# Kernel tuning notes

Measured on AMD Instinct MI355X. Metric: run time of the kernel, lower is better.

## Reference

```python
import jax, jax.numpy as jnp
import numpy as np

B, T, C = 2, 2048, 1024
N_HEAD = 16
HEAD_DIM = C // N_HEAD


def setup_inputs() -> dict:
    key = jax.random.key(0)
    ks = jax.random.split(key, 5)
    s = 0.02
    return {
        "x": jax.random.normal(ks[0], (B, T, C), dtype=jnp.float32),
        "W_kqv": jax.random.normal(ks[1], (C, 3 * C), dtype=jnp.float32) * s,
        "b_kqv": jax.random.normal(ks[2], (3 * C,), dtype=jnp.float32) * s,
        "W_proj": jax.random.normal(ks[3], (C, C), dtype=jnp.float32) * s,
        "b_proj": jax.random.normal(ks[4], (C,), dtype=jnp.float32) * s,
    }


def reference(x, W_kqv, b_kqv, W_proj, b_proj):
    Bx, Tx, Cx = x.shape
    qkv = x @ W_kqv + b_kqv                      # [B, T, 3C]
    q, k, v = jnp.split(qkv, 3, axis=-1)
    # [B, H, T, D]
    q = q.reshape(Bx, Tx, N_HEAD, HEAD_DIM).transpose(0, 2, 1, 3)
    k = k.reshape(Bx, Tx, N_HEAD, HEAD_DIM).transpose(0, 2, 1, 3)
    v = v.reshape(Bx, Tx, N_HEAD, HEAD_DIM).transpose(0, 2, 1, 3)
    scale = 1.0 / jnp.sqrt(jnp.asarray(HEAD_DIM, dtype=x.dtype))
    att = jnp.einsum("bhqd,bhkd->bhqk", q, k) * scale  # [B, H, T, T]
    causal = jnp.tril(jnp.ones((Tx, Tx), dtype=bool))   # [T, T]
    att = jnp.where(causal[None, None], att, jnp.float32(-jnp.inf))
    att = jax.nn.softmax(att, axis=-1)
    y = jnp.einsum("bhqk,bhkd->bhqd", att, v)            # [B, H, T, D]
    y = y.transpose(0, 2, 1, 3).reshape(Bx, Tx, Cx)
    out = y @ W_proj + b_proj
    return out, k, v
```

## Files before the change

kernel.cpp:

```cpp
#include <hip/hip_runtime.h>


#define DEVI __device__ __forceinline__

typedef unsigned short ushort_t;
typedef unsigned long long u64_t;
typedef __attribute__((ext_vector_type(4))) unsigned short us4;
typedef __attribute__((ext_vector_type(8))) unsigned short ushort8;
typedef __attribute__((ext_vector_type(4))) float f32x4;
typedef __attribute__((ext_vector_type(8))) __bf16 bf16x8;

DEVI unsigned short f2bf(float f) {
  union { float f; unsigned int u; } c; c.f = f;
  unsigned int u = c.u;
  unsigned int r = (u + 0x7FFFu + ((u >> 16) & 1u)) >> 16;
  return (unsigned short)r;
}

DEVI float exp2v(float x) {
  float r;
  asm("v_exp_f32 %0, %1\n\ts_nop 0" : "=v"(r) : "v"(x));
  return r;
}

DEVI unsigned int cvtpk(float lo, float hi) {
  unsigned int r;
  asm("v_cvt_pk_bf16_f32 %0, %1, %2" : "=v"(r) : "v"(lo), "v"(hi));
  return r;
}

DEVI f32x4 mfma16(ushort8 a, ushort8 b, f32x4 c) {
  return __builtin_amdgcn_mfma_f32_16x16x32_bf16(
      __builtin_bit_cast(bf16x8, a), __builtin_bit_cast(bf16x8, b), c, 0, 0, 0);
}

typedef const __attribute__((address_space(1))) void* gptr_t;
typedef __attribute__((address_space(3))) void* lptr_t;
#define GLOAD_LDS16(g, l) \
  __builtin_amdgcn_global_load_lds((gptr_t)(g), (lptr_t)(l), 16, 0, 0)

DEVI void bar() {
  asm volatile("" ::: "memory");
  __builtin_amdgcn_s_barrier();
  asm volatile("" ::: "memory");
}
#define VMCNT(n) asm volatile("s_waitcnt vmcnt(" #n ")" ::: "memory")


__global__ void prep_kernel(const float* __restrict__ x,
                            const float* __restrict__ Wk,
                            const float* __restrict__ Wp,
                            ushort_t* __restrict__ Xb,
                            ushort_t* __restrict__ Wkt,
                            ushort_t* __restrict__ Wpt) {
  __shared__ float tile[32][33];
  const int id = blockIdx.x, tid = threadIdx.x;
  if (id < 2048) {
    const int i = id * 256 + tid;
    const f32x4* p = (const f32x4*)x;
    f32x4 a = p[2 * i], b = p[2 * i + 1];
    ushort8 o;
    o[0] = f2bf(a[0]); o[1] = f2bf(a[1]); o[2] = f2bf(a[2]); o[3] = f2bf(a[3]);
    o[4] = f2bf(b[0]); o[5] = f2bf(b[1]); o[6] = f2bf(b[2]); o[7] = f2bf(b[3]);
    ((ushort8*)Xb)[i] = o;
    return;
  }
  const float* in;
  ushort_t* outp;
  int R = 1024, Cin, bx, by;
  if (id < 5120) {
    const int jid = id - 2048;
    bx = jid % 96; by = jid / 96; in = Wk; outp = Wkt; Cin = 3072;
  } else {
    const int jid = id - 5120;
    bx = jid % 32; by = jid / 32; in = Wp; outp = Wpt; Cin = 1024;
  }
  const int c0 = bx * 32, r0 = by * 32;
  const int tx = tid & 31, ty = tid >> 5;
#pragma unroll
  for (int it = 0; it < 4; ++it)
    tile[ty + it * 8][tx] = in[(size_t)(r0 + ty + it * 8) * Cin + c0 + tx];
  __syncthreads();
#pragma unroll
  for (int it = 0; it < 4; ++it)
    outp[(size_t)(c0 + ty + it * 8) * R + r0 + tx] = f2bf(tile[tx][ty + it * 8]);
}


__global__ __launch_bounds__(256) void gemm_bt_kernel(
    const ushort_t* __restrict__ A, const ushort_t* __restrict__ Bt,
    const float* __restrict__ bias, float* __restrict__ outF,
    float* __restrict__ outK, float* __restrict__ outV,
    ushort_t* __restrict__ Qb, ushort_t* __restrict__ Kb, ushort_t* __restrict__ Vb,
    int M, int N, int K, int mode) {
  __shared__ __align__(16) ushort_t As[128 * 64];
  __shared__ __align__(16) ushort_t Bs[128 * 64];
  const int tid = threadIdx.x;
  const int w = tid >> 6, lane = tid & 63;
  const int wr = w >> 1, wc = w & 1;
  const int nby = gridDim.y;
  const int chy = nby >> 3;
  const int orig = blockIdx.x + gridDim.x * blockIdx.y;
  const int xcd = orig & 7, idx = orig >> 3;
  const int by = xcd * chy + (idx % chy);
  const int bx = idx / chy;
  const int m0 = by * 128, n0 = bx * 128;
  const int l15 = lane & 15, lhi = lane >> 4;
  const int rowA = lane >> 3;
  const int sgc = (((lane & 7) ^ ((lane >> 3) & 7)) << 3);

  f32x4 acc[4][4] = {};

  const int nk = K >> 6;
  for (int kt = 0; kt < nk; ++kt) {
    const size_t k0 = (size_t)kt << 6;
    if (kt) bar();
#pragma unroll
    for (int it = 0; it < 4; ++it) {
      const int rbase = (w * 4 + it) * 8;
      GLOAD_LDS16(A + (size_t)(m0 + rbase + rowA) * K + k0 + sgc, &As[rbase * 64]);
      GLOAD_LDS16(Bt + (size_t)(n0 + rbase + rowA) * K + k0 + sgc, &Bs[rbase * 64]);
    }
    VMCNT(0);
    bar();
#pragma unroll
    for (int kk = 0; kk < 2; ++kk) {
      const int gof = (((kk * 4 + lhi) ^ (l15 & 7)) << 3);
      ushort8 a[4], b[4];
#pragma unroll
      for (int i = 0; i < 4; ++i)
        a[i] = *(const ushort8*)&As[(wr * 64 + i * 16 + l15) * 64 + gof];
#pragma unroll
      for (int j = 0; j < 4; ++j)
        b[j] = *(const ushort8*)&Bs[(wc * 64 + j * 16 + l15) * 64 + gof];
#pragma unroll
      for (int i = 0; i < 4; ++i)
#pragma unroll
        for (int j = 0; j < 4; ++j) acc[i][j] = mfma16(a[i], b[j], acc[i][j]);
    }
  }

  const float QSCALE = 0.18033688011112042f;
#pragma unroll
  for (int i = 0; i < 4; ++i) {
#pragma unroll
    for (int j = 0; j < 4; ++j) {
      const int nn = n0 + wc * 64 + j * 16 + l15;
      const float bv = bias[nn];
#pragma unroll
      for (int r = 0; r < 4; ++r) {
        const int mm = m0 + wr * 64 + i * 16 + lhi * 4 + r;
        const float v = acc[i][j][r] + bv;
        if (mode == 0) {
          outF[(size_t)mm * N + nn] = v;
        } else {
          const int bb = mm >> 11, t = mm & 2047;
          const int c = nn & 1023, h = c >> 6, d = c & 63;
          const size_t idx2 = ((size_t)(bb * 16 + h) * 2048 + t) * 64 + d;
          const int sec = nn >> 10;
          if (sec == 0) {
            Qb[idx2] = f2bf(v * QSCALE);
          } else if (sec == 1) {
            outK[idx2] = v; Kb[idx2] = f2bf(v);
          } else {
            outV[idx2] = v; Vb[idx2] = f2bf(v);
          }
        }
      }
    }
  }
}


__global__ __launch_bounds__(256) void gemm_bt64_kernel(
    const ushort_t* __restrict__ A, const ushort_t* __restrict__ Bt,
    const float* __restrict__ bias, float* __restrict__ outF,
    int M, int N, int K) {
  __shared__ __align__(16) ushort_t As[64 * 64];
  __shared__ __align__(16) ushort_t Bs[128 * 64];
  const int tid = threadIdx.x;
  const int w = tid >> 6, lane = tid & 63;
  const int wr = w >> 1, wc = w & 1;
  const int nby = gridDim.y;
  const int chy = nby >> 3;
  const int orig = blockIdx.x + gridDim.x * blockIdx.y;
  const int xcd = orig & 7, idx = orig >> 3;
  const int by = xcd * chy + (idx % chy);
  const int bx = idx / chy;
  const int m0 = by * 64, n0 = bx * 128;
  const int l15 = lane & 15, lhi = lane >> 4;
  const int rowA = lane >> 3;
  const int sgc = (((lane & 7) ^ ((lane >> 3) & 7)) << 3);

  f32x4 acc[2][4] = {};

  const int nk = K >> 6;
  for (int kt = 0; kt < nk; ++kt) {
    const size_t k0 = (size_t)kt << 6;
    if (kt) bar();
#pragma unroll
    for (int it = 0; it < 2; ++it) {
      const int rbase = (w * 2 + it) * 8;
      GLOAD_LDS16(A + (size_t)(m0 + rbase + rowA) * K + k0 + sgc, &As[rbase * 64]);
    }
#pragma unroll
    for (int it = 0; it < 4; ++it) {
      const int rbase = (w * 4 + it) * 8;
      GLOAD_LDS16(Bt + (size_t)(n0 + rbase + rowA) * K + k0 + sgc, &Bs[rbase * 64]);
    }
    VMCNT(0);
    bar();
#pragma unroll
    for (int kk = 0; kk < 2; ++kk) {
      const int gof = (((kk * 4 + lhi) ^ (l15 & 7)) << 3);
      ushort8 a[2], b[4];
#pragma unroll
      for (int i = 0; i < 2; ++i)
        a[i] = *(const ushort8*)&As[(wr * 32 + i * 16 + l15) * 64 + gof];
#pragma unroll
      for (int j = 0; j < 4; ++j)
        b[j] = *(const ushort8*)&Bs[(wc * 64 + j * 16 + l15) * 64 + gof];
#pragma unroll
      for (int i = 0; i < 2; ++i)
#pragma unroll
        for (int j = 0; j < 4; ++j) acc[i][j] = mfma16(a[i], b[j], acc[i][j]);
    }
  }

#pragma unroll
  for (int i = 0; i < 2; ++i) {
#pragma unroll
    for (int j = 0; j < 4; ++j) {
      const int nn = n0 + wc * 64 + j * 16 + l15;
      const float bv = bias[nn];
#pragma unroll
      for (int r = 0; r < 4; ++r) {
        const int mm = m0 + wr * 32 + i * 16 + lhi * 4 + r;
        outF[(size_t)mm * N + nn] = acc[i][j][r] + bv;
      }
    }
  }
}


__global__ __launch_bounds__(512) void attn_kernel(
    const ushort_t* __restrict__ Qb, const ushort_t* __restrict__ Kb,
    const ushort_t* __restrict__ Vb, ushort_t* __restrict__ Yb) {
  __shared__ __align__(16) ushort_t Ks[2][64 * 64];
  __shared__ __align__(16) ushort_t Vt[2][64 * 72];
  __shared__ __align__(16) ushort_t Pl[8 * 16 * 72];
  const int id = blockIdx.x;
  const int xcd = id & 7;
  int qt, bh;
  if (id < 256) {
    const int j = id >> 3;
    bh = xcd + 8 * (j & 3);
    qt = 8 + (j >> 2);
  } else {
    const int j = (id - 256) >> 3;
    bh = xcd + 8 * (j & 3);
    qt = 7 - (j >> 2);
  }
  const int b = bh >> 4, h = bh & 15;
  const int tid = threadIdx.x, w = tid >> 6, lane = tid & 63;
  const int l15 = lane & 15, lhi = lane >> 4;
  const int swzP = 2 * (l15 & 3);
  const size_t base = (size_t)bh * 2048 * 64;
  const float NEG_INF = -__builtin_inff();
  ushort_t* myP = &Pl[w * 16 * 72];

  const int krow = tid >> 3, kg = tid & 7;
  const int ksg = kg ^ (krow & 7);
  const int vd0 = (tid & 15) * 4;
  const int vt0 = (tid >> 4) * 2;

  const int nkt = 2 * qt + 2;
  const int qrow = w * 16 + l15;

  ushort8 qf[2];
  {
    const size_t qrg = base + (size_t)(qt * 128 + qrow) * 64;
    qf[0] = *(const ushort8*)&Qb[qrg + lhi * 8];
    qf[1] = *(const ushort8*)&Qb[qrg + 32 + lhi * 8];
  }
  float m_s = NEG_INF, l_s = 0.f;
  f32x4 o[4] = {};

  {
    GLOAD_LDS16(Kb + base + (size_t)krow * 64 + ksg * 8, &Ks[0][tid * 8]);
    const ushort_t* vp = Vb + base + (size_t)vt0 * 64 + vd0;
    u64_t a = *(const u64_t*)vp;
    u64_t c = *(const u64_t*)(vp + 64);
    us4 av = __builtin_bit_cast(us4, a);
    us4 cv = __builtin_bit_cast(us4, c);
#pragma unroll
    for (int i = 0; i < 4; ++i) {
      const int d = vd0 + i;
      const int scg = (vt0 >> 3) ^ ((d >> 3) & 7);
      unsigned int wv = (unsigned int)av[i] | ((unsigned int)cv[i] << 16);
      *(unsigned int*)&Vt[0][d * 72 + scg * 8 + (vt0 & 7)] = wv;
    }
  }
  __syncthreads();

  for (int kt = 0; kt < nkt; ++kt) {
    const int cur = kt & 1, nxt = cur ^ 1;
    const bool pf = (kt + 1 < nkt);
    u64_t va = 0, vc = 0;
    if (pf) {
      const size_t tb = base + (size_t)(kt + 1) * 64 * 64;
      GLOAD_LDS16(Kb + tb + (size_t)krow * 64 + ksg * 8, &Ks[nxt][tid * 8]);
      const ushort_t* vp = Vb + tb + (size_t)vt0 * 64 + vd0;
      va = *(const u64_t*)vp;
      vc = *(const u64_t*)(vp + 64);
    }

    f32x4 s[4] = {};
#pragma unroll
    for (int kk = 0; kk < 2; ++kk) {
#pragma unroll
      for (int j = 0; j < 4; ++j) {
        const int g = (kk * 4 + lhi) ^ (l15 & 7);
        ushort8 kb = *(const ushort8*)&Ks[cur][(j * 16 + l15) * 64 + g * 8];
        s[j] = mfma16(kb, qf[kk], s[j]);
      }
    }
    if (64 * kt + 63 > 128 * qt + w * 16) {
      const int delta = 128 * qt + qrow - 64 * kt;
#pragma unroll
      for (int j = 0; j < 4; ++j)
#pragma unroll
        for (int r = 0; r < 4; ++r)
          if ((j * 16 + lhi * 4 + r) > delta) s[j][r] = NEG_INF;
    }

    float pmax = s[0][0];
#pragma unroll
    for (int j = 0; j < 4; ++j)
#pragma unroll
      for (int r = 0; r < 4; ++r) pmax = fmaxf(pmax, s[j][r]);
    pmax = fmaxf(pmax, __shfl_xor(pmax, 16));
    pmax = fmaxf(pmax, __shfl_xor(pmax, 32));
    if (__any(pmax - m_s > 8.0f)) {
      const float mnew = fmaxf(m_s, pmax);
      const float al = exp2v(m_s - mnew);
      m_s = mnew;
      l_s *= al;
#pragma unroll
      for (int df = 0; df < 4; ++df)
#pragma unroll
        for (int r = 0; r < 4; ++r) o[df][r] *= al;
    }
    float rsum = 0.f;
#pragma unroll
    for (int j = 0; j < 4; ++j)
#pragma unroll
      for (int r = 0; r < 4; ++r) {
        const float pe = exp2v(s[j][r] - m_s);
        s[j][r] = pe;
        rsum += pe;
      }
    rsum += __shfl_xor(rsum, 16);
    rsum += __shfl_xor(rsum, 32);
    l_s += rsum;

#pragma unroll
    for (int j = 0; j < 4; ++j) {
      const unsigned int w0 = cvtpk(s[j][0], s[j][1]);
      const unsigned int w1 = cvtpk(s[j][2], s[j][3]);
      const u64_t dw = (u64_t)w0 | ((u64_t)w1 << 32);
      const int cg = j * 2 + (lhi >> 1);
      *(u64_t*)&myP[l15 * 72 + ((cg ^ swzP) << 3) + ((lhi & 1) << 2)] = dw;
    }

#pragma unroll
    for (int kk = 0; kk < 2; ++kk) {
      ushort8 pa = *(const ushort8*)&myP[l15 * 72 + (((kk * 4 + lhi) ^ swzP) << 3)];
#pragma unroll
      for (int df = 0; df < 4; ++df) {
        const int r = df * 16 + l15;
        const int g = (kk * 4 + lhi) ^ ((r >> 3) & 7);
        ushort8 vb = *(const ushort8*)&Vt[cur][r * 72 + g * 8];
        o[df] = mfma16(vb, pa, o[df]);
      }
    }

    if (pf) {
      us4 av = __builtin_bit_cast(us4, va);
      us4 cv = __builtin_bit_cast(us4, vc);
#pragma unroll
      for (int i = 0; i < 4; ++i) {
        const int d = vd0 + i;
        const int scg = (vt0 >> 3) ^ ((d >> 3) & 7);
        unsigned int wv = (unsigned int)av[i] | ((unsigned int)cv[i] << 16);
        *(unsigned int*)&Vt[nxt][d * 72 + scg * 8 + (vt0 & 7)] = wv;
      }
    }
    __syncthreads();
  }

  const float inv = 1.0f / l_s;
  const size_t yrow = (size_t)(b * 2048 + qt * 128 + qrow) * 1024 + h * 64;
#pragma unroll
  for (int df = 0; df < 4; ++df) {
    us4 ov;
#pragma unroll
    for (int r = 0; r < 4; ++r) ov[r] = f2bf(o[df][r] * inv);
    *(us4*)&Yb[yrow + df * 16 + lhi * 4] = ov;
  }
}


extern "C" void kernel_launch(void* const* d_in, const int* in_sizes, int n_in,
                              void* d_out, int out_size, void* d_ws, size_t ws_size,
                              hipStream_t stream) {
  const float* x      = (const float*)d_in[0];
  const float* W_kqv  = (const float*)d_in[1];
  const float* b_kqv  = (const float*)d_in[2];
  const float* W_proj = (const float*)d_in[3];
  const float* b_proj = (const float*)d_in[4];
  float* out  = (float*)d_out;
  float* outK = out + 4194304;
  float* outV = out + 8388608;

  char* ws = (char*)d_ws;
  ushort_t* Xb  = (ushort_t*)(ws);
  ushort_t* Wkt = (ushort_t*)(ws + ((size_t)8 << 20));
  ushort_t* Wpt = (ushort_t*)(ws + ((size_t)14 << 20));
  ushort_t* Qb  = (ushort_t*)(ws + ((size_t)16 << 20));
  ushort_t* Kb  = (ushort_t*)(ws + ((size_t)24 << 20));
  ushort_t* Vb  = (ushort_t*)(ws + ((size_t)32 << 20));
  ushort_t* Yb  = Xb;

  prep_kernel<<<6144, 256, 0, stream>>>(x, W_kqv, W_proj, Xb, Wkt, Wpt);
  gemm_bt_kernel<<<dim3(24, 32), 256, 0, stream>>>(
      Xb, Wkt, b_kqv, nullptr, outK, outV, Qb, Kb, Vb, 4096, 3072, 1024, 1);
  attn_kernel<<<512, 512, 0, stream>>>(Qb, Kb, Vb, Yb);
  gemm_bt64_kernel<<<dim3(8, 64), 256, 0, stream>>>(
      Yb, Wpt, b_proj, out, 4096, 1024, 1024);
}
```

Before: 106.7 us.

## Halve attention block to 4 waves, each handling two 16-row query groups

The attention kernel now runs 256 threads per block instead of 512. Each wave owns 32 query rows as two 16-row groups, so every K and V fragment read from LDS feeds two MFMAs, and the wave keeps two sets of softmax state. The K/V tile loads are split across two iterations per thread, and the V transpose swizzle changes from (d>>3) to (d>>2). The aim is to cut LDS read traffic per MFMA, at the cost of more registers per wave and fewer waves per block to hide latency.

```diff
diff --git a/kernel.cpp b/kernel.cpp
--- a/kernel.cpp
+++ b/kernel.cpp
@@ -243,7 +243,7 @@
 }
 
 
-__global__ __launch_bounds__(512) void attn_kernel(
+__global__ __launch_bounds__(256) void attn_kernel(
     const ushort_t* __restrict__ Qb, const ushort_t* __restrict__ Kb,
     const ushort_t* __restrict__ Vb, ushort_t* __restrict__ Yb) {
   __shared__ __align__(16) ushort_t Ks[2][64 * 64];
@@ -267,38 +267,46 @@
   const int swzP = 2 * (l15 & 3);
   const size_t base = (size_t)bh * 2048 * 64;
   const float NEG_INF = -__builtin_inff();
-  ushort_t* myP = &Pl[w * 16 * 72];
-
-  const int krow = tid >> 3, kg = tid & 7;
-  const int ksg = kg ^ (krow & 7);
+  ushort_t* myP = &Pl[w * 2 * 16 * 72];
+
   const int vd0 = (tid & 15) * 4;
-  const int vt0 = (tid >> 4) * 2;
+  const int vt0b = (tid >> 4) * 2;
 
   const int nkt = 2 * qt + 2;
-  const int qrow = w * 16 + l15;
-
-  ushort8 qf[2];
+
+  ushort8 qf[2][2];
+#pragma unroll
+  for (int qg = 0; qg < 2; ++qg) {
+    const size_t qrg = base + (size_t)(qt * 128 + w * 32 + qg * 16 + l15) * 64;
+    qf[qg][0] = *(const ushort8*)&Qb[qrg + lhi * 8];
+    qf[qg][1] = *(const ushort8*)&Qb[qrg + 32 + lhi * 8];
+  }
+  float m_s[2] = {NEG_INF, NEG_INF}, l_s[2] = {0.f, 0.f};
+  f32x4 o[2][4] = {};
+
   {
-    const size_t qrg = base + (size_t)(qt * 128 + qrow) * 64;
-    qf[0] = *(const ushort8*)&Qb[qrg + lhi * 8];
-    qf[1] = *(const ushort8*)&Qb[qrg + 32 + lhi * 8];
-  }
-  float m_s = NEG_INF, l_s = 0.f;
-  f32x4 o[4] = {};
-
-  {
-    GLOAD_LDS16(Kb + base + (size_t)krow * 64 + ksg * 8, &Ks[0][tid * 8]);
-    const ushort_t* vp = Vb + base + (size_t)vt0 * 64 + vd0;
-    u64_t a = *(const u64_t*)vp;
-    u64_t c = *(const u64_t*)(vp + 64);
-    us4 av = __builtin_bit_cast(us4, a);
-    us4 cv = __builtin_bit_cast(us4, c);
-#pragma unroll
-    for (int i = 0; i < 4; ++i) {
-      const int d = vd0 + i;
-      const int scg = (vt0 >> 3) ^ ((d >> 3) & 7);
-      unsigned int wv = (unsigned int)av[i] | ((unsigned int)cv[i] << 16);
-      *(unsigned int*)&Vt[0][d * 72 + scg * 8 + (vt0 & 7)] = wv;
+#pragma unroll
+    for (int it = 0; it < 2; ++it) {
+      const int chunk = tid + it * 256;
+      const int row = chunk >> 3, g = chunk & 7;
+      const int sg = g ^ (row & 7);
+      GLOAD_LDS16(Kb + base + (size_t)row * 64 + sg * 8, &Ks[0][chunk * 8]);
+    }
+#pragma unroll
+    for (int it = 0; it < 2; ++it) {
+      const int t0 = vt0b + it * 32;
+      const ushort_t* vp = Vb + base + (size_t)t0 * 64 + vd0;
+      u64_t a = *(const u64_t*)vp;
+      u64_t c = *(const u64_t*)(vp + 64);
+      us4 av = __builtin_bit_cast(us4, a);
+      us4 cv = __builtin_bit_cast(us4, c);
+#pragma unroll
+      for (int i = 0; i < 4; ++i) {
+        const int d = vd0 + i;
+        const int scg = (t0 >> 3) ^ ((d >> 2) & 7);
+        unsigned int wv = (unsigned int)av[i] | ((unsigned int)cv[i] << 16);
+        *(unsigned int*)&Vt[0][d * 72 + scg * 8 + (t0 & 7)] = wv;
+      }
     }
   }
   __syncthreads();
@@ -306,107 +314,133 @@
   for (int kt = 0; kt < nkt; ++kt) {
     const int cur = kt & 1, nxt = cur ^ 1;
     const bool pf = (kt + 1 < nkt);
-    u64_t va = 0, vc = 0;
+    u64_t va[2], vc[2];
     if (pf) {
       const size_t tb = base + (size_t)(kt + 1) * 64 * 64;
-      GLOAD_LDS16(Kb + tb + (size_t)krow * 64 + ksg * 8, &Ks[nxt][tid * 8]);
-      const ushort_t* vp = Vb + tb + (size_t)vt0 * 64 + vd0;
-      va = *(const u64_t*)vp;
-      vc = *(const u64_t*)(vp + 64);
-    }
-
-    f32x4 s[4] = {};
+#pragma unroll
+      for (int it = 0; it < 2; ++it) {
+        const int chunk = tid + it * 256;
+        const int row = chunk >> 3, g = chunk & 7;
+        const int sg = g ^ (row & 7);
+        GLOAD_LDS16(Kb + tb + (size_t)row * 64 + sg * 8, &Ks[nxt][chunk * 8]);
+      }
+#pragma unroll
+      for (int it = 0; it < 2; ++it) {
+        const int t0 = vt0b + it * 32;
+        const ushort_t* vp = Vb + tb + (size_t)t0 * 64 + vd0;
+        va[it] = *(const u64_t*)vp;
+        vc[it] = *(const u64_t*)(vp + 64);
+      }
+    }
+
+    f32x4 s[2][4] = {};
 #pragma unroll
     for (int kk = 0; kk < 2; ++kk) {
 #pragma unroll
       for (int j = 0; j < 4; ++j) {
         const int g = (kk * 4 + lhi) ^ (l15 & 7);
         ushort8 kb = *(const ushort8*)&Ks[cur][(j * 16 + l15) * 64 + g * 8];
-        s[j] = mfma16(kb, qf[kk], s[j]);
-      }
-    }
-    if (64 * kt + 63 > 128 * qt + w * 16) {
-      const int delta = 128 * qt + qrow - 64 * kt;
+        s[0][j] = mfma16(kb, qf[0][kk], s[0][j]);
+        s[1][j] = mfma16(kb, qf[1][kk], s[1][j]);
+      }
+    }
+
+#pragma unroll
+    for (int qg = 0; qg < 2; ++qg) {
+      const int qrow = w * 32 + qg * 16 + l15;
+      if (64 * kt + 63 > 128 * qt + w * 32 + qg * 16) {
+        const int delta = 128 * qt + qrow - 64 * kt;
+#pragma unroll
+        for (int j = 0; j < 4; ++j)
+#pragma unroll
+          for (int r = 0; r < 4; ++r)
+            if ((j * 16 + lhi * 4 + r) > delta) s[qg][j][r] = NEG_INF;
+      }
+      float pmax = s[qg][0][0];
 #pragma unroll
       for (int j = 0; j < 4; ++j)
 #pragma unroll
-        for (int r = 0; r < 4; ++r)
-          if ((j * 16 + lhi * 4 + r) > delta) s[j][r] = NEG_INF;
-    }
-
-    float pmax = s[0][0];
-#pragma unroll
-    for (int j = 0; j < 4; ++j)
-#pragma unroll
-      for (int r = 0; r < 4; ++r) pmax = fmaxf(pmax, s[j][r]);
-    pmax = fmaxf(pmax, __shfl_xor(pmax, 16));
-    pmax = fmaxf(pmax, __shfl_xor(pmax, 32));
-    if (__any(pmax - m_s > 8.0f)) {
-      const float mnew = fmaxf(m_s, pmax);
-      const float al = exp2v(m_s - mnew);
-      m_s = mnew;
-      l_s *= al;
-#pragma unroll
-      for (int df = 0; df < 4; ++df)
-#pragma unroll
-        for (int r = 0; r < 4; ++r) o[df][r] *= al;
-    }
-    float rsum = 0.f;
-#pragma unroll
-    for (int j = 0; j < 4; ++j)
-#pragma unroll
-      for (int r = 0; r < 4; ++r) {
-        const float pe = exp2v(s[j][r] - m_s);
-        s[j][r] = pe;
-        rsum += pe;
-      }
-    rsum += __shfl_xor(rsum, 16);
-    rsum += __shfl_xor(rsum, 32);
-    l_s += rsum;
-
-#pragma unroll
-    for (int j = 0; j < 4; ++j) {
-      const unsigned int w0 = cvtpk(s[j][0], s[j][1]);
-      const unsigned int w1 = cvtpk(s[j][2], s[j][3]);
-      const u64_t dw = (u64_t)w0 | ((u64_t)w1 << 32);
-      const int cg = j * 2 + (lhi >> 1);
-      *(u64_t*)&myP[l15 * 72 + ((cg ^ swzP) << 3) + ((lhi & 1) << 2)] = dw;
+        for (int r = 0; r < 4; ++r) pmax = fmaxf(pmax, s[qg][j][r]);
+      pmax = fmaxf(pmax, __shfl_xor(pmax, 16));
+      pmax = fmaxf(pmax, __shfl_xor(pmax, 32));
+      if (__any(pmax - m_s[qg] > 8.0f)) {
+        const float mnew = fmaxf(m_s[qg], pmax);
+        const float al = exp2v(m_s[qg] - mnew);
+        m_s[qg] = mnew;
+        l_s[qg] *= al;
+#pragma unroll
+        for (int df = 0; df < 4; ++df)
+#pragma unroll
+          for (int r = 0; r < 4; ++r) o[qg][df][r] *= al;
+      }
+      float rsum = 0.f;
+#pragma unroll
+      for (int j = 0; j < 4; ++j)
+#pragma unroll
+        for (int r = 0; r < 4; ++r) {
+          const float pe = exp2v(s[qg][j][r] - m_s[qg]);
+          s[qg][j][r] = pe;
+          rsum += pe;
+        }
+      rsum += __shfl_xor(rsum, 16);
+      rsum += __shfl_xor(rsum, 32);
+      l_s[qg] += rsum;
+
+      ushort_t* pq = myP + qg * 16 * 72;
+#pragma unroll
+      for (int j = 0; j < 4; ++j) {
+        const unsigned int w0 = cvtpk(s[qg][j][0], s[qg][j][1]);
+        const unsigned int w1 = cvtpk(s[qg][j][2], s[qg][j][3]);
+        const u64_t dw = (u64_t)w0 | ((u64_t)w1 << 32);
+        const int cg = j * 2 + (lhi >> 1);
+        *(u64_t*)&pq[l15 * 72 + ((cg ^ swzP) << 3) + ((lhi & 1) << 2)] = dw;
+      }
     }
 
 #pragma unroll
     for (int kk = 0; kk < 2; ++kk) {
-      ushort8 pa = *(const ushort8*)&myP[l15 * 72 + (((kk * 4 + lhi) ^ swzP) << 3)];
+      ushort8 pa0 = *(const ushort8*)&myP[l15 * 72 + (((kk * 4 + lhi) ^ swzP) << 3)];
+      ushort8 pa1 = *(const ushort8*)&myP[16 * 72 + l15 * 72 + (((kk * 4 + lhi) ^ swzP) << 3)];
 #pragma unroll
       for (int df = 0; df < 4; ++df) {
         const int r = df * 16 + l15;
-        const int g = (kk * 4 + lhi) ^ ((r >> 3) & 7);
+        const int g = (kk * 4 + lhi) ^ ((r >> 2) & 7);
         ushort8 vb = *(const ushort8*)&Vt[cur][r * 72 + g * 8];
-        o[df] = mfma16(vb, pa, o[df]);
+        o[0][df] = mfma16(vb, pa0, o[0][df]);
+        o[1][df] = mfma16(vb, pa1, o[1][df]);
       }
     }
 
     if (pf) {
-      us4 av = __builtin_bit_cast(us4, va);
-      us4 cv = __builtin_bit_cast(us4, vc);
-#pragma unroll
-      for (int i = 0; i < 4; ++i) {
-        const int d = vd0 + i;
-        const int scg = (vt0 >> 3) ^ ((d >> 3) & 7);
-        unsigned int wv = (unsigned int)av[i] | ((unsigned int)cv[i] << 16);
-        *(unsigned int*)&Vt[nxt][d * 72 + scg * 8 + (vt0 & 7)] = wv;
+#pragma unroll
+      for (int it = 0; it < 2; ++it) {
+        const int t0 = vt0b + it * 32;
+        us4 av = __builtin_bit_cast(us4, va[it]);
+        us4 cv = __builtin_bit_cast(us4, vc[it]);
+#pragma unroll
+        for (int i = 0; i < 4; ++i) {
+          const int d = vd0 + i;
+          const int scg = (t0 >> 3) ^ ((d >> 2) & 7);
+          unsigned int wv = (unsigned int)av[i] | ((unsigned int)cv[i] << 16);
+          *(unsigned int*)&Vt[nxt][d * 72 + scg * 8 + (t0 & 7)] = wv;
+        }
       }
     }
     __syncthreads();
   }
 
-  const float inv = 1.0f / l_s;
-  const size_t yrow = (size_t)(b * 2048 + qt * 128 + qrow) * 1024 + h * 64;
-#pragma unroll
-  for (int df = 0; df < 4; ++df) {
-    us4 ov;
-#pragma unroll
-    for (int r = 0; r < 4; ++r) ov[r] = f2bf(o[df][r] * inv);
-    *(us4*)&Yb[yrow + df * 16 + lhi * 4] = ov;
+#pragma unroll
+  for (int qg = 0; qg < 2; ++qg) {
+    const float inv = 1.0f / l_s[qg];
+    const size_t yrow =
+        (size_t)(b * 2048 + qt * 128 + w * 32 + qg * 16 + l15) * 1024 + h * 64;
+#pragma unroll
+    for (int df = 0; df < 4; ++df) {
+      us4 ov;
+#pragma unroll
+      for (int r = 0; r < 4; ++r) ov[r] = f2bf(o[qg][df][r] * inv);
+      *(us4*)&Yb[yrow + df * 16 + lhi * 4] = ov;
+    }
   }
 }
 
@@ -435,7 +469,7 @@
   prep_kernel<<<6144, 256, 0, stream>>>(x, W_kqv, W_proj, Xb, Wkt, Wpt);
   gemm_bt_kernel<<<dim3(24, 32), 256, 0, stream>>>(
       Xb, Wkt, b_kqv, nullptr, outK, outV, Qb, Kb, Vb, 4096, 3072, 1024, 1);
-  attn_kernel<<<512, 512, 0, stream>>>(Qb, Kb, Vb, Yb);
+  attn_kernel<<<512, 256, 0, stream>>>(Qb, Kb, Vb, Yb);
   gemm_bt64_kernel<<<dim3(8, 64), 256, 0, stream>>>(
       Yb, Wpt, b_proj, out, 4096, 1024, 1024);
 }
```

Result: slower. 124.3 us (+16.5%).

## Deepen attention K/V prefetch to two tiles ahead with triple-buffered K

Applied to the files above, without the earlier changes.

K tiles move into a three-slot LDS ring and V tiles are held in two register sets, so loads are issued two iterations ahead instead of one. Explicit vmcnt/lgkmcnt waits and a raw barrier replace __syncthreads, which lets the global loads stay in flight across an iteration. This hides more global-load latency but uses extra LDS and registers, which may lower occupancy.

```diff
diff --git a/kernel.cpp b/kernel.cpp
--- a/kernel.cpp
+++ b/kernel.cpp
@@ -45,6 +45,7 @@
   asm volatile("" ::: "memory");
 }
 #define VMCNT(n) asm volatile("s_waitcnt vmcnt(" #n ")" ::: "memory")
+#define LGKM0 asm volatile("s_waitcnt lgkmcnt(0)" ::: "memory")
 
 
 __global__ void prep_kernel(const float* __restrict__ x,
@@ -246,7 +247,7 @@
 __global__ __launch_bounds__(512) void attn_kernel(
     const ushort_t* __restrict__ Qb, const ushort_t* __restrict__ Kb,
     const ushort_t* __restrict__ Vb, ushort_t* __restrict__ Yb) {
-  __shared__ __align__(16) ushort_t Ks[2][64 * 64];
+  __shared__ __align__(16) ushort_t Ks[3 * 64 * 64];
   __shared__ __align__(16) ushort_t Vt[2][64 * 72];
   __shared__ __align__(16) ushort_t Pl[8 * 16 * 72];
   const int id = blockIdx.x;
@@ -286,33 +287,41 @@
   float m_s = NEG_INF, l_s = 0.f;
   f32x4 o[4] = {};
 
+  u64_t vaA, vcA, vaB, vcB;
+
   {
-    GLOAD_LDS16(Kb + base + (size_t)krow * 64 + ksg * 8, &Ks[0][tid * 8]);
-    const ushort_t* vp = Vb + base + (size_t)vt0 * 64 + vd0;
-    u64_t a = *(const u64_t*)vp;
-    u64_t c = *(const u64_t*)(vp + 64);
-    us4 av = __builtin_bit_cast(us4, a);
-    us4 cv = __builtin_bit_cast(us4, c);
+    GLOAD_LDS16(Kb + base + (size_t)krow * 64 + ksg * 8, &Ks[tid * 8]);
+    const ushort_t* vp0 = Vb + base + (size_t)vt0 * 64 + vd0;
+    vaA = *(const u64_t*)vp0;
+    vcA = *(const u64_t*)(vp0 + 64);
+    GLOAD_LDS16(Kb + base + 4096 + (size_t)krow * 64 + ksg * 8,
+                &Ks[4096 + tid * 8]);
+    const ushort_t* vp1 = Vb + base + 4096 + (size_t)vt0 * 64 + vd0;
+    vaB = *(const u64_t*)vp1;
+    vcB = *(const u64_t*)(vp1 + 64);
+    VMCNT(3);
+    us4 av = __builtin_bit_cast(us4, vaA), cv = __builtin_bit_cast(us4, vcA);
 #pragma unroll
     for (int i = 0; i < 4; ++i) {
       const int d = vd0 + i;
       const int scg = (vt0 >> 3) ^ ((d >> 3) & 7);
-      unsigned int wv = (unsigned int)av[i] | ((unsigned int)cv[i] << 16);
-      *(unsigned int*)&Vt[0][d * 72 + scg * 8 + (vt0 & 7)] = wv;
-    }
-  }
-  __syncthreads();
-
-  for (int kt = 0; kt < nkt; ++kt) {
-    const int cur = kt & 1, nxt = cur ^ 1;
-    const bool pf = (kt + 1 < nkt);
-    u64_t va = 0, vc = 0;
-    if (pf) {
-      const size_t tb = base + (size_t)(kt + 1) * 64 * 64;
-      GLOAD_LDS16(Kb + tb + (size_t)krow * 64 + ksg * 8, &Ks[nxt][tid * 8]);
+      *(unsigned int*)&Vt[0][d * 72 + scg * 8 + (vt0 & 7)] =
+          (unsigned int)av[i] | ((unsigned int)cv[i] << 16);
+    }
+    LGKM0;
+    bar();
+  }
+
+  auto step = [&](int t, int kr, int kf, int vtR,
+                  u64_t& fa, u64_t& fc, u64_t& wa, u64_t& wc)
+      __attribute__((always_inline)) {
+    const bool issue = (t + 2 < nkt);
+    if (issue) {
+      const size_t tb = base + (size_t)(t + 2) * 4096;
+      GLOAD_LDS16(Kb + tb + (size_t)krow * 64 + ksg * 8, &Ks[kf + tid * 8]);
       const ushort_t* vp = Vb + tb + (size_t)vt0 * 64 + vd0;
-      va = *(const u64_t*)vp;
-      vc = *(const u64_t*)(vp + 64);
+      fa = *(const u64_t*)vp;
+      fc = *(const u64_t*)(vp + 64);
     }
 
     f32x4 s[4] = {};
@@ -321,12 +330,12 @@
 #pragma unroll
       for (int j = 0; j < 4; ++j) {
         const int g = (kk * 4 + lhi) ^ (l15 & 7);
-        ushort8 kb = *(const ushort8*)&Ks[cur][(j * 16 + l15) * 64 + g * 8];
+        ushort8 kb = *(const ushort8*)&Ks[kr + (j * 16 + l15) * 64 + g * 8];
         s[j] = mfma16(kb, qf[kk], s[j]);
       }
     }
-    if (64 * kt + 63 > 128 * qt + w * 16) {
-      const int delta = 128 * qt + qrow - 64 * kt;
+    if (64 * t + 63 > 128 * qt + w * 16) {
+      const int delta = 128 * qt + qrow - 64 * t;
 #pragma unroll
       for (int j = 0; j < 4; ++j)
 #pragma unroll
@@ -380,23 +389,40 @@
       for (int df = 0; df < 4; ++df) {
         const int r = df * 16 + l15;
         const int g = (kk * 4 + lhi) ^ ((r >> 3) & 7);
-        ushort8 vb = *(const ushort8*)&Vt[cur][r * 72 + g * 8];
+        ushort8 vb = *(const ushort8*)&Vt[vtR][r * 72 + g * 8];
         o[df] = mfma16(vb, pa, o[df]);
       }
     }
 
-    if (pf) {
-      us4 av = __builtin_bit_cast(us4, va);
-      us4 cv = __builtin_bit_cast(us4, vc);
+    if (issue) {
+      VMCNT(3);
+    } else {
+      VMCNT(0);
+    }
+    if (t + 1 < nkt) {
+      us4 av = __builtin_bit_cast(us4, wa), cv = __builtin_bit_cast(us4, wc);
 #pragma unroll
       for (int i = 0; i < 4; ++i) {
         const int d = vd0 + i;
         const int scg = (vt0 >> 3) ^ ((d >> 3) & 7);
-        unsigned int wv = (unsigned int)av[i] | ((unsigned int)cv[i] << 16);
-        *(unsigned int*)&Vt[nxt][d * 72 + scg * 8 + (vt0 & 7)] = wv;
-      }
-    }
-    __syncthreads();
+        *(unsigned int*)&Vt[vtR ^ 1][d * 72 + scg * 8 + (vt0 & 7)] =
+            (unsigned int)av[i] | ((unsigned int)cv[i] << 16);
+      }
+    }
+    LGKM0;
+    bar();
+  };
+
+  int t = 0, kr = 0, kf = 8192;
+  for (;;) {
+    step(t, kr, kf, 0, vaA, vcA, vaB, vcB);
+    if (++t == nkt) break;
+    kr = (kr == 8192) ? 0 : kr + 4096;
+    kf = (kf == 8192) ? 0 : kf + 4096;
+    step(t, kr, kf, 1, vaB, vcB, vaA, vcA);
+    if (++t == nkt) break;
+    kr = (kr == 8192) ? 0 : kr + 4096;
+    kf = (kf == 8192) ? 0 : kf + 4096;
   }
 
   const float inv = 1.0f / l_s;
```

Result: no change. 107.3 us (+0.5%).

## Switch attention to 32x32 MFMA with register-resident P via permlane swap

Applied to the files above, without the earlier changes.

Rewrites the attention kernel to use 32x32x16 bf16 MFMA with 4 waves per block, each handling 32 query rows, instead of 8 waves on 16-row tiles. The softmax probabilities are packed into B-operand fragments in registers with v_permlane32_swap, removing the per-wave LDS round trip for P. K and V tile loads are split across fewer threads. This is meant to cut LDS traffic and instruction overhead, at the cost of more registers per thread and fewer waves per block to hide latency.

```diff
diff --git a/kernel.cpp b/kernel.cpp
--- a/kernel.cpp
+++ b/kernel.cpp
@@ -8,7 +8,9 @@
 typedef __attribute__((ext_vector_type(4))) unsigned short us4;
 typedef __attribute__((ext_vector_type(8))) unsigned short ushort8;
 typedef __attribute__((ext_vector_type(4))) float f32x4;
+typedef __attribute__((ext_vector_type(16))) float f32x16;
 typedef __attribute__((ext_vector_type(8))) __bf16 bf16x8;
+typedef __attribute__((ext_vector_type(4))) unsigned int u32x4;
 
 DEVI unsigned short f2bf(float f) {
   union { float f; unsigned int u; } c; c.f = f;
@@ -29,8 +31,17 @@
   return r;
 }
 
+DEVI void plswap(unsigned int& a, unsigned int& b) {
+  asm volatile("v_permlane32_swap_b32 %0, %1" : "+v"(a), "+v"(b));
+}
+
 DEVI f32x4 mfma16(ushort8 a, ushort8 b, f32x4 c) {
   return __builtin_amdgcn_mfma_f32_16x16x32_bf16(
+      __builtin_bit_cast(bf16x8, a), __builtin_bit_cast(bf16x8, b), c, 0, 0, 0);
+}
+
+DEVI f32x16 mfma32(ushort8 a, ushort8 b, f32x16 c) {
+  return __builtin_amdgcn_mfma_f32_32x32x16_bf16(
       __builtin_bit_cast(bf16x8, a), __builtin_bit_cast(bf16x8, b), c, 0, 0, 0);
 }
 
@@ -243,12 +254,11 @@
 }
 
 
-__global__ __launch_bounds__(512) void attn_kernel(
+__global__ __launch_bounds__(256) void attn_kernel(
     const ushort_t* __restrict__ Qb, const ushort_t* __restrict__ Kb,
     const ushort_t* __restrict__ Vb, ushort_t* __restrict__ Yb) {
   __shared__ __align__(16) ushort_t Ks[2][64 * 64];
   __shared__ __align__(16) ushort_t Vt[2][64 * 72];
-  __shared__ __align__(16) ushort_t Pl[8 * 16 * 72];
   const int id = blockIdx.x;
   const int xcd = id & 7;
   int qt, bh;
@@ -263,42 +273,49 @@
   }
   const int b = bh >> 4, h = bh & 15;
   const int tid = threadIdx.x, w = tid >> 6, lane = tid & 63;
-  const int l15 = lane & 15, lhi = lane >> 4;
-  const int swzP = 2 * (l15 & 3);
+  const int l31 = lane & 31, lhi1 = lane >> 5;
   const size_t base = (size_t)bh * 2048 * 64;
   const float NEG_INF = -__builtin_inff();
-  ushort_t* myP = &Pl[w * 16 * 72];
-
-  const int krow = tid >> 3, kg = tid & 7;
-  const int ksg = kg ^ (krow & 7);
+
   const int vd0 = (tid & 15) * 4;
-  const int vt0 = (tid >> 4) * 2;
+  const int vt0b = (tid >> 4) * 2;
 
   const int nkt = 2 * qt + 2;
-  const int qrow = w * 16 + l15;
-
-  ushort8 qf[2];
+  const int qg = 128 * qt + w * 32 + l31;
+
+  ushort8 qf[4];
   {
-    const size_t qrg = base + (size_t)(qt * 128 + qrow) * 64;
-    qf[0] = *(const ushort8*)&Qb[qrg + lhi * 8];
-    qf[1] = *(const ushort8*)&Qb[qrg + 32 + lhi * 8];
+    const size_t qrg = base + (size_t)qg * 64;
+#pragma unroll
+    for (int ch = 0; ch < 4; ++ch)
+      qf[ch] = *(const ushort8*)&Qb[qrg + ch * 16 + lhi1 * 8];
   }
   float m_s = NEG_INF, l_s = 0.f;
-  f32x4 o[4] = {};
+  f32x16 o0 = {}, o1 = {};
 
   {
-    GLOAD_LDS16(Kb + base + (size_t)krow * 64 + ksg * 8, &Ks[0][tid * 8]);
-    const ushort_t* vp = Vb + base + (size_t)vt0 * 64 + vd0;
-    u64_t a = *(const u64_t*)vp;
-    u64_t c = *(const u64_t*)(vp + 64);
-    us4 av = __builtin_bit_cast(us4, a);
-    us4 cv = __builtin_bit_cast(us4, c);
-#pragma unroll
-    for (int i = 0; i < 4; ++i) {
-      const int d = vd0 + i;
-      const int scg = (vt0 >> 3) ^ ((d >> 3) & 7);
-      unsigned int wv = (unsigned int)av[i] | ((unsigned int)cv[i] << 16);
-      *(unsigned int*)&Vt[0][d * 72 + scg * 8 + (vt0 & 7)] = wv;
+#pragma unroll
+    for (int it = 0; it < 2; ++it) {
+      const int chunk = tid + it * 256;
+      const int row = chunk >> 3, g = chunk & 7;
+      const int sg = g ^ (row & 7);
+      GLOAD_LDS16(Kb + base + (size_t)row * 64 + sg * 8, &Ks[0][chunk * 8]);
+    }
+#pragma unroll
+    for (int it = 0; it < 2; ++it) {
+      const int t0 = vt0b + it * 32;
+      const ushort_t* vp = Vb + base + (size_t)t0 * 64 + vd0;
+      u64_t a = *(const u64_t*)vp;
+      u64_t c = *(const u64_t*)(vp + 64);
+      us4 av = __builtin_bit_cast(us4, a);
+      us4 cv = __builtin_bit_cast(us4, c);
+#pragma unroll
+      for (int i = 0; i < 4; ++i) {
+        const int d = vd0 + i;
+        const int scg = (t0 >> 3) ^ ((d >> 2) & 7);
+        unsigned int wv = (unsigned int)av[i] | ((unsigned int)cv[i] << 16);
+        *(unsigned int*)&Vt[0][d * 72 + scg * 8 + (t0 & 7)] = wv;
+      }
     }
   }
   __syncthreads();
@@ -306,40 +323,48 @@
   for (int kt = 0; kt < nkt; ++kt) {
     const int cur = kt & 1, nxt = cur ^ 1;
     const bool pf = (kt + 1 < nkt);
-    u64_t va = 0, vc = 0;
+    u64_t va0, vc0, va1, vc1;
     if (pf) {
-      const size_t tb = base + (size_t)(kt + 1) * 64 * 64;
-      GLOAD_LDS16(Kb + tb + (size_t)krow * 64 + ksg * 8, &Ks[nxt][tid * 8]);
-      const ushort_t* vp = Vb + tb + (size_t)vt0 * 64 + vd0;
-      va = *(const u64_t*)vp;
-      vc = *(const u64_t*)(vp + 64);
-    }
-
-    f32x4 s[4] = {};
-#pragma unroll
-    for (int kk = 0; kk < 2; ++kk) {
-#pragma unroll
-      for (int j = 0; j < 4; ++j) {
-        const int g = (kk * 4 + lhi) ^ (l15 & 7);
-        ushort8 kb = *(const ushort8*)&Ks[cur][(j * 16 + l15) * 64 + g * 8];
-        s[j] = mfma16(kb, qf[kk], s[j]);
-      }
-    }
-    if (64 * kt + 63 > 128 * qt + w * 16) {
-      const int delta = 128 * qt + qrow - 64 * kt;
-#pragma unroll
-      for (int j = 0; j < 4; ++j)
-#pragma unroll
-        for (int r = 0; r < 4; ++r)
-          if ((j * 16 + lhi * 4 + r) > delta) s[j][r] = NEG_INF;
-    }
-
-    float pmax = s[0][0];
-#pragma unroll
-    for (int j = 0; j < 4; ++j)
-#pragma unroll
-      for (int r = 0; r < 4; ++r) pmax = fmaxf(pmax, s[j][r]);
-    pmax = fmaxf(pmax, __shfl_xor(pmax, 16));
+      const size_t tb = base + (size_t)(kt + 1) * 4096;
+#pragma unroll
+      for (int it = 0; it < 2; ++it) {
+        const int chunk = tid + it * 256;
+        const int row = chunk >> 3, g = chunk & 7;
+        const int sg = g ^ (row & 7);
+        GLOAD_LDS16(Kb + tb + (size_t)row * 64 + sg * 8, &Ks[nxt][chunk * 8]);
+      }
+      const ushort_t* vp0 = Vb + tb + (size_t)vt0b * 64 + vd0;
+      va0 = *(const u64_t*)vp0;
+      vc0 = *(const u64_t*)(vp0 + 64);
+      const ushort_t* vp1 = Vb + tb + (size_t)(vt0b + 32) * 64 + vd0;
+      va1 = *(const u64_t*)vp1;
+      vc1 = *(const u64_t*)(vp1 + 64);
+    }
+
+    f32x16 s0 = {}, s1 = {};
+#pragma unroll
+    for (int ch = 0; ch < 4; ++ch) {
+      const int gp = ((2 * ch + lhi1) ^ (l31 & 7)) << 3;
+      ushort8 k0 = *(const ushort8*)&Ks[cur][l31 * 64 + gp];
+      ushort8 k1 = *(const ushort8*)&Ks[cur][(32 + l31) * 64 + gp];
+      s0 = mfma32(k0, qf[ch], s0);
+      s1 = mfma32(k1, qf[ch], s1);
+    }
+
+    if (64 * kt + 63 > 128 * qt + w * 32) {
+#pragma unroll
+      for (int r = 0; r < 16; ++r) {
+        const int kvb = 64 * kt + (r & 3) + 8 * (r >> 2) + 4 * lhi1;
+        if (kvb > qg) s0[r] = NEG_INF;
+        if (kvb + 32 > qg) s1[r] = NEG_INF;
+      }
+    }
+
+    float pmax = s0[0];
+#pragma unroll
+    for (int r = 1; r < 16; ++r) pmax = fmaxf(pmax, s0[r]);
+#pragma unroll
+    for (int r = 0; r < 16; ++r) pmax = fmaxf(pmax, s1[r]);
     pmax = fmaxf(pmax, __shfl_xor(pmax, 32));
     if (__any(pmax - m_s > 8.0f)) {
       const float mnew = fmaxf(m_s, pmax);
@@ -347,66 +372,92 @@
       m_s = mnew;
       l_s *= al;
 #pragma unroll
-      for (int df = 0; df < 4; ++df)
-#pragma unroll
-        for (int r = 0; r < 4; ++r) o[df][r] *= al;
+      for (int r = 0; r < 16; ++r) { o0[r] *= al; o1[r] *= al; }
     }
     float rsum = 0.f;
 #pragma unroll
-    for (int j = 0; j < 4; ++j)
-#pragma unroll
-      for (int r = 0; r < 4; ++r) {
-        const float pe = exp2v(s[j][r] - m_s);
-        s[j][r] = pe;
-        rsum += pe;
-      }
-    rsum += __shfl_xor(rsum, 16);
+    for (int r = 0; r < 16; ++r) {
+      s0[r] = exp2v(s0[r] - m_s);
+      rsum += s0[r];
+    }
+#pragma unroll
+    for (int r = 0; r < 16; ++r) {
+      s1[r] = exp2v(s1[r] - m_s);
+      rsum += s1[r];
+    }
     rsum += __shfl_xor(rsum, 32);
     l_s += rsum;
 
-#pragma unroll
-    for (int j = 0; j < 4; ++j) {
-      const unsigned int w0 = cvtpk(s[j][0], s[j][1]);
-      const unsigned int w1 = cvtpk(s[j][2], s[j][3]);
-      const u64_t dw = (u64_t)w0 | ((u64_t)w1 << 32);
-      const int cg = j * 2 + (lhi >> 1);
-      *(u64_t*)&myP[l15 * 72 + ((cg ^ swzP) << 3) + ((lhi & 1) << 2)] = dw;
-    }
-
-#pragma unroll
-    for (int kk = 0; kk < 2; ++kk) {
-      ushort8 pa = *(const ushort8*)&myP[l15 * 72 + (((kk * 4 + lhi) ^ swzP) << 3)];
-#pragma unroll
-      for (int df = 0; df < 4; ++df) {
-        const int r = df * 16 + l15;
-        const int g = (kk * 4 + lhi) ^ ((r >> 3) & 7);
-        ushort8 vb = *(const ushort8*)&Vt[cur][r * 72 + g * 8];
-        o[df] = mfma16(vb, pa, o[df]);
+    ushort8 pfr[4];
+#pragma unroll
+    for (int kc = 0; kc < 4; ++kc) {
+      const int hh = (kc & 1) * 8;
+      unsigned int a0, a1, b0, b1;
+      if (kc < 2) {
+        a0 = cvtpk(s0[hh + 0], s0[hh + 1]);
+        a1 = cvtpk(s0[hh + 2], s0[hh + 3]);
+        b0 = cvtpk(s0[hh + 4], s0[hh + 5]);
+        b1 = cvtpk(s0[hh + 6], s0[hh + 7]);
+      } else {
+        a0 = cvtpk(s1[hh + 0], s1[hh + 1]);
+        a1 = cvtpk(s1[hh + 2], s1[hh + 3]);
+        b0 = cvtpk(s1[hh + 4], s1[hh + 5]);
+        b1 = cvtpk(s1[hh + 6], s1[hh + 7]);
+      }
+      plswap(a0, b0);
+      plswap(a1, b1);
+      u32x4 fr;
+      fr[0] = a0; fr[1] = a1; fr[2] = b0; fr[3] = b1;
+      pfr[kc] = __builtin_bit_cast(ushort8, fr);
+    }
+
+#pragma unroll
+    for (int kc = 0; kc < 4; ++kc) {
+      {
+        const int d = l31;
+        const int gv = ((2 * kc + lhi1) ^ ((d >> 2) & 7)) << 3;
+        ushort8 vf = *(const ushort8*)&Vt[cur][d * 72 + gv];
+        o0 = mfma32(vf, pfr[kc], o0);
+      }
+      {
+        const int d = 32 + l31;
+        const int gv = ((2 * kc + lhi1) ^ ((d >> 2) & 7)) << 3;
+        ushort8 vf = *(const ushort8*)&Vt[cur][d * 72 + gv];
+        o1 = mfma32(vf, pfr[kc], o1);
       }
     }
 
     if (pf) {
-      us4 av = __builtin_bit_cast(us4, va);
-      us4 cv = __builtin_bit_cast(us4, vc);
+      us4 av0 = __builtin_bit_cast(us4, va0), cv0 = __builtin_bit_cast(us4, vc0);
+      us4 av1 = __builtin_bit_cast(us4, va1), cv1 = __builtin_bit_cast(us4, vc1);
 #pragma unroll
       for (int i = 0; i < 4; ++i) {
         const int d = vd0 + i;
-        const int scg = (vt0 >> 3) ^ ((d >> 3) & 7);
-        unsigned int wv = (unsigned int)av[i] | ((unsigned int)cv[i] << 16);
-        *(unsigned int*)&Vt[nxt][d * 72 + scg * 8 + (vt0 & 7)] = wv;
+        const int key = ((d >> 2) & 7);
+        const int scg0 = (vt0b >> 3) ^ key;
+        const int scg1 = ((vt0b + 32) >> 3) ^ key;
+        *(unsigned int*)&Vt[nxt][d * 72 + scg0 * 8 + (vt0b & 7)] =
+            (unsigned int)av0[i] | ((unsigned int)cv0[i] << 16);
+        *(unsigned int*)&Vt[nxt][d * 72 + scg1 * 8 + (vt0b & 7)] =
+            (unsigned int)av1[i] | ((unsigned int)cv1[i] << 16);
       }
     }
     __syncthreads();
   }
 
   const float inv = 1.0f / l_s;
-  const size_t yrow = (size_t)(b * 2048 + qt * 128 + qrow) * 1024 + h * 64;
-#pragma unroll
-  for (int df = 0; df < 4; ++df) {
-    us4 ov;
-#pragma unroll
-    for (int r = 0; r < 4; ++r) ov[r] = f2bf(o[df][r] * inv);
-    *(us4*)&Yb[yrow + df * 16 + lhi * 4] = ov;
+  const size_t yrow = (size_t)(b * 2048 + qg) * 1024 + h * 64;
+#pragma unroll
+  for (int rq = 0; rq < 4; ++rq) {
+    us4 ov0, ov1;
+#pragma unroll
+    for (int e = 0; e < 4; ++e) {
+      ov0[e] = f2bf(o0[rq * 4 + e] * inv);
+      ov1[e] = f2bf(o1[rq * 4 + e] * inv);
+    }
+    const int dof = rq * 8 + lhi1 * 4;
+    *(us4*)&Yb[yrow + dof] = ov0;
+    *(us4*)&Yb[yrow + 32 + dof] = ov1;
   }
 }
 
@@ -435,7 +486,7 @@
   prep_kernel<<<6144, 256, 0, stream>>>(x, W_kqv, W_proj, Xb, Wkt, Wpt);
   gemm_bt_kernel<<<dim3(24, 32), 256, 0, stream>>>(
       Xb, Wkt, b_kqv, nullptr, outK, outV, Qb, Kb, Vb, 4096, 3072, 1024, 1);
-  attn_kernel<<<512, 512, 0, stream>>>(Qb, Kb, Vb, Yb);
+  attn_kernel<<<512, 256, 0, stream>>>(Qb, Kb, Vb, Yb);
   gemm_bt64_kernel<<<dim3(8, 64), 256, 0, stream>>>(
       Yb, Wpt, b_proj, out, 4096, 1024, 1024);
 }
```

New measurement: 116.5 us. 9.2% more time.
